# Kernel tuning notes

Measured on AMD Instinct MI355X. Metric: run time of the kernel, lower is better.

## Reference

```python
import jax, jax.numpy as jnp
import numpy as np


def _binarize(v):
    # Straight-through-estimator binarization (standard in BNN repos):
    # forward = sign(v) (mapped to +/-1), backward = identity.
    s = jnp.where(v >= 0, 1.0, -1.0).astype(v.dtype)
    return v + jax.lax.stop_gradient(s - v)


def setup_inputs() -> dict:
    key = jax.random.key(0)
    k1, k2 = jax.random.split(key)
    N, D_IN, D_OUT = 8192, 4096, 4096
    x = jax.random.normal(k1, (N, D_IN), dtype=jnp.float32)
    # xavier/glorot uniform init for weight [d_in, num_out]
    limit = np.sqrt(6.0 / (D_IN + D_OUT)).astype(np.float32)
    weight = jax.random.uniform(k2, (D_IN, D_OUT), dtype=jnp.float32, minval=-limit, maxval=limit)
    return {"x": x, "weight": weight}


def reference(x, weight):
    xb = _binarize(x)          # binarize_input=True
    wb = _binarize(weight)
    return jnp.matmul(xb, wb)  # [N, num_out]
```

## Files before the change

kernel.cpp:

```cpp
#include <hip/hip_runtime.h>
#include <stdint.h>


#define DIN  4096
#define DOUT 4096
#define BM   256
#define BN   256
#define BK   128
#define NT   (DIN / BK)

typedef __attribute__((ext_vector_type(4))) int v4i;
typedef unsigned int u32;

__device__ __forceinline__ void cp16(void* lds, const void* g) {
    __builtin_amdgcn_global_load_lds((const __attribute__((address_space(1))) u32*)g,
                                     (__attribute__((address_space(3))) u32*)lds,
                                     16, 0, 0);
}

__global__ __launch_bounds__(256) void pack_x_i8(const float* __restrict__ x,
                                                 signed char* __restrict__ xb) {
    size_t i = (size_t)blockIdx.x * 256 + threadIdx.x;
    float4 v = ((const float4*)x)[i];
    char4 s;
    s.x = v.x >= 0.f ? 1 : -1;
    s.y = v.y >= 0.f ? 1 : -1;
    s.z = v.z >= 0.f ? 1 : -1;
    s.w = v.w >= 0.f ? 1 : -1;
    ((char4*)xb)[i] = s;
}

__global__ __launch_bounds__(256) void pack_wT_i8(const float* __restrict__ w,
                                                  signed char* __restrict__ wbT) {
    __shared__ signed char tile[64][80];
    const int k0 = blockIdx.y * 64, n0 = blockIdx.x * 64;
    const int t = threadIdx.x;
    const int j  = t & 63;
    const int i0 = t >> 6;
    #pragma unroll
    for (int s = 0; s < 16; s++) {
        int i = i0 + s * 4;
        float v = w[(size_t)(k0 + i) * DOUT + n0 + j];
        tile[j][i] = v >= 0.f ? 1 : -1;
    }
    __syncthreads();
    const int n  = t >> 2;
    const int kk = (t & 3) * 16;
    v4i val = *(const v4i*)&tile[n][kk];
    *(v4i*)&wbT[(size_t)(n0 + n) * DIN + k0 + kk] = val;
}

__global__ __launch_bounds__(512, 2) void bgemm_i8(const signed char* __restrict__ xb,
                                                   const signed char* __restrict__ wbT,
                                                   float* __restrict__ out) {
    __shared__ __align__(16) signed char As[2][BM * BK];
    __shared__ __align__(16) signed char Bs[2][BN * BK];

    const int t = threadIdx.x;
    const int l = t & 63;
    const int w = t >> 6;
    const int wr = w & 1;
    const int wc = w >> 1;
    const int m = l & 15, quad = l >> 4;
    const int sw = (m & 7) << 4;

    const int bm = blockIdx.y * BM, bn = blockIdx.x * BN;
    const signed char* gA = xb  + (size_t)bm * DIN;
    const signed char* gB = wbT + (size_t)bn * DIN;

    const int    sr   = t >> 3;
    const size_t soff = (size_t)sr * DIN + (((t & 7) ^ (sr & 7)) * 16);
    const int    ldst = t * 16;

#define SU(lbuf, gmat, r0, kk) \
    cp16(&(lbuf)[(r0) * BK + ldst], (gmat) + (size_t)(r0) * DIN + (size_t)(kk) + soff)

    v4i acc[8][4];
    #pragma unroll
    for (int i = 0; i < 8; i++)
        #pragma unroll
        for (int j = 0; j < 4; j++) {
            v4i z = {0, 0, 0, 0};
            acc[i][j] = z;
        }

    SU(Bs[0], gB, 0, 0);   SU(Bs[0], gB, 64, 0);
    SU(Bs[0], gB, 128, 0); SU(Bs[0], gB, 192, 0);
    SU(As[0], gA, 0, 0);   SU(As[0], gA, 128, 0);
    SU(As[0], gA, 64, 0);  SU(As[0], gA, 192, 0);
    asm volatile("s_waitcnt vmcnt(0)" ::: "memory");
    __builtin_amdgcn_s_barrier();

    for (int kt = 0; kt < NT - 1; ++kt) {
        const int cur = kt & 1, nxt = cur ^ 1;
        const int kk = (kt + 1) * BK;
        #pragma unroll
        for (int p = 0; p < 4; ++p) {
            v4i a[2][2], b[2][4];
            #pragma unroll
            for (int i = 0; i < 2; ++i) {
                const signed char* rp = &As[cur][(wr * 128 + (2 * p + i) * 16 + m) * BK];
                a[0][i] = *(const v4i*)(rp + ((quad * 16) ^ sw));
                a[1][i] = *(const v4i*)(rp + ((64 + quad * 16) ^ sw));
            }
            #pragma unroll
            for (int j = 0; j < 4; ++j) {
                const signed char* rp = &Bs[cur][(wc * 64 + j * 16 + m) * BK];
                b[0][j] = *(const v4i*)(rp + ((quad * 16) ^ sw));
                b[1][j] = *(const v4i*)(rp + ((64 + quad * 16) ^ sw));
            }
            if (p == 0) { SU(Bs[nxt], gB, 0, kk);   SU(Bs[nxt], gB, 64, kk); }
            if (p == 1) { SU(Bs[nxt], gB, 128, kk); SU(Bs[nxt], gB, 192, kk); }
            if (p == 2) { SU(As[nxt], gA, 0, kk);   SU(As[nxt], gA, 128, kk); }
            if (p == 3) { SU(As[nxt], gA, 64, kk);  SU(As[nxt], gA, 192, kk); }

            __builtin_amdgcn_s_barrier();
            asm volatile("s_waitcnt lgkmcnt(0)" ::: "memory");
            __builtin_amdgcn_sched_barrier(0);
            __builtin_amdgcn_s_setprio(1);
            #pragma unroll
            for (int ks = 0; ks < 2; ++ks)
                #pragma unroll
                for (int i = 0; i < 2; ++i)
                    #pragma unroll
                    for (int j = 0; j < 4; ++j)
                        acc[2 * p + i][j] = __builtin_amdgcn_mfma_i32_16x16x64_i8(
                            a[ks][i], b[ks][j], acc[2 * p + i][j], 0, 0, 0);
            __builtin_amdgcn_s_setprio(0);
            __builtin_amdgcn_sched_barrier(0);
            if (p == 1) asm volatile("s_waitcnt vmcnt(4)" ::: "memory");
            if (p == 3) asm volatile("s_waitcnt vmcnt(2)" ::: "memory");
            __builtin_amdgcn_s_barrier();
        }
    }

    {
        const int cur = (NT - 1) & 1;
        #pragma unroll
        for (int p = 0; p < 4; ++p) {
            v4i a[2][2], b[2][4];
            #pragma unroll
            for (int i = 0; i < 2; ++i) {
                const signed char* rp = &As[cur][(wr * 128 + (2 * p + i) * 16 + m) * BK];
                a[0][i] = *(const v4i*)(rp + ((quad * 16) ^ sw));
                a[1][i] = *(const v4i*)(rp + ((64 + quad * 16) ^ sw));
            }
            #pragma unroll
            for (int j = 0; j < 4; ++j) {
                const signed char* rp = &Bs[cur][(wc * 64 + j * 16 + m) * BK];
                b[0][j] = *(const v4i*)(rp + ((quad * 16) ^ sw));
                b[1][j] = *(const v4i*)(rp + ((64 + quad * 16) ^ sw));
            }
            __builtin_amdgcn_s_barrier();
            asm volatile("s_waitcnt lgkmcnt(0)" ::: "memory");
            __builtin_amdgcn_sched_barrier(0);
            __builtin_amdgcn_s_setprio(1);
            #pragma unroll
            for (int ks = 0; ks < 2; ++ks)
                #pragma unroll
                for (int i = 0; i < 2; ++i)
                    #pragma unroll
                    for (int j = 0; j < 4; ++j)
                        acc[2 * p + i][j] = __builtin_amdgcn_mfma_i32_16x16x64_i8(
                            a[ks][i], b[ks][j], acc[2 * p + i][j], 0, 0, 0);
            __builtin_amdgcn_s_setprio(0);
            __builtin_amdgcn_sched_barrier(0);
            if (p == 1) asm volatile("s_waitcnt vmcnt(0)" ::: "memory");
            __builtin_amdgcn_s_barrier();
        }
    }
#undef SU

    #pragma unroll
    for (int i = 0; i < 8; i++) {
        int row0 = bm + wr * 128 + i * 16 + quad * 4;
        #pragma unroll
        for (int j = 0; j < 4; j++) {
            int col = bn + wc * 64 + j * 16 + m;
            #pragma unroll
            for (int r = 0; r < 4; r++)
                out[(size_t)(row0 + r) * DOUT + col] = (float)acc[i][j][r];
        }
    }
}

extern "C" void kernel_launch(void* const* d_in, const int* in_sizes, int n_in,
                              void* d_out, int out_size, void* d_ws, size_t ws_size,
                              hipStream_t stream) {
    const float* x = (const float*)d_in[0];
    const float* w = (const float*)d_in[1];
    float* out = (float*)d_out;
    const int N = in_sizes[0] / DIN;

    signed char* xb  = (signed char*)d_ws;
    signed char* wbT = (signed char*)d_ws + (size_t)N * DIN;

    pack_x_i8<<<(N * DIN) / 1024, 256, 0, stream>>>(x, xb);
    pack_wT_i8<<<dim3(DOUT / 64, DIN / 64), 256, 0, stream>>>(w, wbT);
    bgemm_i8<<<dim3(DOUT / BN, N / BM), 512, 0, stream>>>(xb, wbT, out);
}
```

Measured before the change: 406.0 us.

## Switch GEMM to 32x32x32 int8 MFMA, swizzle tiles, vectorize packing kernels

The GEMM inner loop moves from 16x16x64 to 32x32x32 int8 MFMA tiles, and the B fragments are loaded once per k-tile and reused across both A phases. This halves the number of phases and cuts LDS reads. Block indices are remapped so that consecutive blocks share tiles in L2. The pack_x kernel now handles 16 elements per thread, the pack_wT kernel uses float4 loads, and the initial wait is loosened to vmcnt(2). The risks are higher register pressure from the 16-wide accumulators and a less coalesced output store pattern.

Result: no change. 399.4 us (-1.6%).

```diff
diff --git a/kernel.cpp b/kernel.cpp
--- a/kernel.cpp
+++ b/kernel.cpp
@@ -9,7 +9,8 @@
 #define BK   128
 #define NT   (DIN / BK)
 
-typedef __attribute__((ext_vector_type(4))) int v4i;
+typedef __attribute__((ext_vector_type(4)))  int v4i;
+typedef __attribute__((ext_vector_type(16))) int v16i;
 typedef unsigned int u32;
 
 __device__ __forceinline__ void cp16(void* lds, const void* g) {
@@ -20,14 +21,19 @@
 
 __global__ __launch_bounds__(256) void pack_x_i8(const float* __restrict__ x,
                                                  signed char* __restrict__ xb) {
-    size_t i = (size_t)blockIdx.x * 256 + threadIdx.x;
-    float4 v = ((const float4*)x)[i];
-    char4 s;
-    s.x = v.x >= 0.f ? 1 : -1;
-    s.y = v.y >= 0.f ? 1 : -1;
-    s.z = v.z >= 0.f ? 1 : -1;
-    s.w = v.w >= 0.f ? 1 : -1;
-    ((char4*)xb)[i] = s;
+    size_t g = (size_t)blockIdx.x * 256 + threadIdx.x;
+    const float4* xv = (const float4*)x + g * 4;
+    v4i o;
+    #pragma unroll
+    for (int q = 0; q < 4; q++) {
+        float4 v = xv[q];
+        int c0 = v.x >= 0.f ? 1 : 0xFF;
+        int c1 = v.y >= 0.f ? 1 : 0xFF;
+        int c2 = v.z >= 0.f ? 1 : 0xFF;
+        int c3 = v.w >= 0.f ? 1 : 0xFF;
+        o[q] = c0 | (c1 << 8) | (c2 << 16) | (c3 << 24);
+    }
+    ((v4i*)xb)[g] = o;
 }
 
 __global__ __launch_bounds__(256) void pack_wT_i8(const float* __restrict__ w,
@@ -35,13 +41,16 @@
     __shared__ signed char tile[64][80];
     const int k0 = blockIdx.y * 64, n0 = blockIdx.x * 64;
     const int t = threadIdx.x;
-    const int j  = t & 63;
-    const int i0 = t >> 6;
-    #pragma unroll
-    for (int s = 0; s < 16; s++) {
-        int i = i0 + s * 4;
-        float v = w[(size_t)(k0 + i) * DOUT + n0 + j];
-        tile[j][i] = v >= 0.f ? 1 : -1;
+    const int j4 = (t & 15) * 4;
+    const int i0 = t >> 4;
+    #pragma unroll
+    for (int s = 0; s < 4; s++) {
+        int i = i0 + s * 16;
+        float4 v = *(const float4*)&w[(size_t)(k0 + i) * DOUT + n0 + j4];
+        tile[j4 + 0][i] = v.x >= 0.f ? 1 : -1;
+        tile[j4 + 1][i] = v.y >= 0.f ? 1 : -1;
+        tile[j4 + 2][i] = v.z >= 0.f ? 1 : -1;
+        tile[j4 + 3][i] = v.w >= 0.f ? 1 : -1;
     }
     __syncthreads();
     const int n  = t >> 2;
@@ -61,10 +70,14 @@
     const int w = t >> 6;
     const int wr = w & 1;
     const int wc = w >> 1;
-    const int m = l & 15, quad = l >> 4;
-    const int sw = (m & 7) << 4;
-
-    const int bm = blockIdx.y * BM, bn = blockIdx.x * BN;
+    const int lm = l & 31;
+    const int hi = l >> 5;
+    const int sw = (lm & 7) << 4;
+
+    const int fid = blockIdx.y * gridDim.x + blockIdx.x;
+    const int swz = (fid & 7) * 64 + (fid >> 3);
+    const int bm = (swz >> 4) * BM, bn = (swz & 15) * BN;
+
     const signed char* gA = xb  + (size_t)bm * DIN;
     const signed char* gB = wbT + (size_t)bn * DIN;
 
@@ -75,61 +88,68 @@
 #define SU(lbuf, gmat, r0, kk) \
     cp16(&(lbuf)[(r0) * BK + ldst], (gmat) + (size_t)(r0) * DIN + (size_t)(kk) + soff)
 
-    v4i acc[8][4];
-    #pragma unroll
-    for (int i = 0; i < 8; i++)
-        #pragma unroll
-        for (int j = 0; j < 4; j++) {
-            v4i z = {0, 0, 0, 0};
-            acc[i][j] = z;
-        }
+    v16i acc[4][2];
+    #pragma unroll
+    for (int i = 0; i < 4; i++)
+        #pragma unroll
+        for (int j = 0; j < 2; j++)
+            #pragma unroll
+            for (int r = 0; r < 16; r++)
+                acc[i][j][r] = 0;
 
     SU(Bs[0], gB, 0, 0);   SU(Bs[0], gB, 64, 0);
     SU(Bs[0], gB, 128, 0); SU(Bs[0], gB, 192, 0);
     SU(As[0], gA, 0, 0);   SU(As[0], gA, 128, 0);
     SU(As[0], gA, 64, 0);  SU(As[0], gA, 192, 0);
-    asm volatile("s_waitcnt vmcnt(0)" ::: "memory");
+    asm volatile("s_waitcnt vmcnt(2)" ::: "memory");
     __builtin_amdgcn_s_barrier();
+
+    v4i b[2][4];
 
     for (int kt = 0; kt < NT - 1; ++kt) {
         const int cur = kt & 1, nxt = cur ^ 1;
         const int kk = (kt + 1) * BK;
         #pragma unroll
-        for (int p = 0; p < 4; ++p) {
-            v4i a[2][2], b[2][4];
+        for (int p = 0; p < 2; ++p) {
+            v4i a[2][4];
             #pragma unroll
             for (int i = 0; i < 2; ++i) {
-                const signed char* rp = &As[cur][(wr * 128 + (2 * p + i) * 16 + m) * BK];
-                a[0][i] = *(const v4i*)(rp + ((quad * 16) ^ sw));
-                a[1][i] = *(const v4i*)(rp + ((64 + quad * 16) ^ sw));
-            }
-            #pragma unroll
-            for (int j = 0; j < 4; ++j) {
-                const signed char* rp = &Bs[cur][(wc * 64 + j * 16 + m) * BK];
-                b[0][j] = *(const v4i*)(rp + ((quad * 16) ^ sw));
-                b[1][j] = *(const v4i*)(rp + ((64 + quad * 16) ^ sw));
-            }
-            if (p == 0) { SU(Bs[nxt], gB, 0, kk);   SU(Bs[nxt], gB, 64, kk); }
-            if (p == 1) { SU(Bs[nxt], gB, 128, kk); SU(Bs[nxt], gB, 192, kk); }
-            if (p == 2) { SU(As[nxt], gA, 0, kk);   SU(As[nxt], gA, 128, kk); }
-            if (p == 3) { SU(As[nxt], gA, 64, kk);  SU(As[nxt], gA, 192, kk); }
+                const signed char* rp = &As[cur][(wr * 128 + (2 * p + i) * 32 + lm) * BK];
+                #pragma unroll
+                for (int ks = 0; ks < 4; ++ks)
+                    a[i][ks] = *(const v4i*)(rp + ((ks * 32 + hi * 16) ^ sw));
+            }
+            if (p == 0) {
+                #pragma unroll
+                for (int j = 0; j < 2; ++j) {
+                    const signed char* rp = &Bs[cur][(wc * 64 + j * 32 + lm) * BK];
+                    #pragma unroll
+                    for (int ks = 0; ks < 4; ++ks)
+                        b[j][ks] = *(const v4i*)(rp + ((ks * 32 + hi * 16) ^ sw));
+                }
+                SU(Bs[nxt], gB, 0, kk);   SU(Bs[nxt], gB, 64, kk);
+                SU(Bs[nxt], gB, 128, kk); SU(Bs[nxt], gB, 192, kk);
+            } else {
+                SU(As[nxt], gA, 0, kk);   SU(As[nxt], gA, 128, kk);
+                SU(As[nxt], gA, 64, kk);  SU(As[nxt], gA, 192, kk);
+            }
 
             __builtin_amdgcn_s_barrier();
             asm volatile("s_waitcnt lgkmcnt(0)" ::: "memory");
             __builtin_amdgcn_sched_barrier(0);
             __builtin_amdgcn_s_setprio(1);
             #pragma unroll
-            for (int ks = 0; ks < 2; ++ks)
+            for (int ks = 0; ks < 4; ++ks)
                 #pragma unroll
                 for (int i = 0; i < 2; ++i)
                     #pragma unroll
-                    for (int j = 0; j < 4; ++j)
-                        acc[2 * p + i][j] = __builtin_amdgcn_mfma_i32_16x16x64_i8(
-                            a[ks][i], b[ks][j], acc[2 * p + i][j], 0, 0, 0);
+                    for (int j = 0; j < 2; ++j)
+                        acc[2 * p + i][j] = __builtin_amdgcn_mfma_i32_32x32x32_i8(
+                            a[i][ks], b[j][ks], acc[2 * p + i][j], 0, 0, 0);
             __builtin_amdgcn_s_setprio(0);
             __builtin_amdgcn_sched_barrier(0);
-            if (p == 1) asm volatile("s_waitcnt vmcnt(4)" ::: "memory");
-            if (p == 3) asm volatile("s_waitcnt vmcnt(2)" ::: "memory");
+            if (p == 0) asm volatile("s_waitcnt vmcnt(4)" ::: "memory");
+            else        asm volatile("s_waitcnt vmcnt(2)" ::: "memory");
             __builtin_amdgcn_s_barrier();
         }
     }
@@ -137,49 +157,54 @@
     {
         const int cur = (NT - 1) & 1;
         #pragma unroll
-        for (int p = 0; p < 4; ++p) {
-            v4i a[2][2], b[2][4];
+        for (int p = 0; p < 2; ++p) {
+            v4i a[2][4];
             #pragma unroll
             for (int i = 0; i < 2; ++i) {
-                const signed char* rp = &As[cur][(wr * 128 + (2 * p + i) * 16 + m) * BK];
-                a[0][i] = *(const v4i*)(rp + ((quad * 16) ^ sw));
-                a[1][i] = *(const v4i*)(rp + ((64 + quad * 16) ^ sw));
-            }
-            #pragma unroll
-            for (int j = 0; j < 4; ++j) {
-                const signed char* rp = &Bs[cur][(wc * 64 + j * 16 + m) * BK];
-                b[0][j] = *(const v4i*)(rp + ((quad * 16) ^ sw));
-                b[1][j] = *(const v4i*)(rp + ((64 + quad * 16) ^ sw));
+                const signed char* rp = &As[cur][(wr * 128 + (2 * p + i) * 32 + lm) * BK];
+                #pragma unroll
+                for (int ks = 0; ks < 4; ++ks)
+                    a[i][ks] = *(const v4i*)(rp + ((ks * 32 + hi * 16) ^ sw));
+            }
+            if (p == 0) {
+                #pragma unroll
+                for (int j = 0; j < 2; ++j) {
+                    const signed char* rp = &Bs[cur][(wc * 64 + j * 32 + lm) * BK];
+                    #pragma unroll
+                    for (int ks = 0; ks < 4; ++ks)
+                        b[j][ks] = *(const v4i*)(rp + ((ks * 32 + hi * 16) ^ sw));
+                }
             }
             __builtin_amdgcn_s_barrier();
             asm volatile("s_waitcnt lgkmcnt(0)" ::: "memory");
             __builtin_amdgcn_sched_barrier(0);
             __builtin_amdgcn_s_setprio(1);
             #pragma unroll
-            for (int ks = 0; ks < 2; ++ks)
+            for (int ks = 0; ks < 4; ++ks)
                 #pragma unroll
                 for (int i = 0; i < 2; ++i)
                     #pragma unroll
-                    for (int j = 0; j < 4; ++j)
-                        acc[2 * p + i][j] = __builtin_amdgcn_mfma_i32_16x16x64_i8(
-                            a[ks][i], b[ks][j], acc[2 * p + i][j], 0, 0, 0);
+                    for (int j = 0; j < 2; ++j)
+                        acc[2 * p + i][j] = __builtin_amdgcn_mfma_i32_32x32x32_i8(
+                            a[i][ks], b[j][ks], acc[2 * p + i][j], 0, 0, 0);
             __builtin_amdgcn_s_setprio(0);
             __builtin_amdgcn_sched_barrier(0);
-            if (p == 1) asm volatile("s_waitcnt vmcnt(0)" ::: "memory");
+            if (p == 0) asm volatile("s_waitcnt vmcnt(0)" ::: "memory");
             __builtin_amdgcn_s_barrier();
         }
     }
 #undef SU
 
     #pragma unroll
-    for (int i = 0; i < 8; i++) {
-        int row0 = bm + wr * 128 + i * 16 + quad * 4;
-        #pragma unroll
-        for (int j = 0; j < 4; j++) {
-            int col = bn + wc * 64 + j * 16 + m;
-            #pragma unroll
-            for (int r = 0; r < 4; r++)
-                out[(size_t)(row0 + r) * DOUT + col] = (float)acc[i][j][r];
+    for (int f = 0; f < 4; f++) {
+        #pragma unroll
+        for (int g = 0; g < 2; g++) {
+            int col = bn + wc * 64 + g * 32 + lm;
+            #pragma unroll
+            for (int r = 0; r < 16; r++) {
+                int row = bm + wr * 128 + f * 32 + (r & 3) + 8 * (r >> 2) + 4 * hi;
+                out[(size_t)row * DOUT + col] = (float)acc[f][g][r];
+            }
         }
     }
 }
@@ -195,7 +220,7 @@
     signed char* xb  = (signed char*)d_ws;
     signed char* wbT = (signed char*)d_ws + (size_t)N * DIN;
 
-    pack_x_i8<<<(N * DIN) / 1024, 256, 0, stream>>>(x, xb);
+    pack_x_i8<<<(N * DIN) / (16 * 256), 256, 0, stream>>>(x, xb);
     pack_wT_i8<<<dim3(DOUT / 64, DIN / 64), 256, 0, stream>>>(w, wbT);
     bgemm_i8<<<dim3(DOUT / BN, N / BM), 512, 0, stream>>>(xb, wbT, out);
 }
```
